# Kernel optimization log

Hardware: AMD Instinct MI355X
Metric: run time of the kernel (lower is better)

Reference implementation:

```python
import jax, jax.numpy as jnp
import numpy as np

HEADS = 8
DIM_HEAD = 64
SCALE = DIM_HEAD ** -0.5


def setup_inputs() -> dict:
    key = jax.random.key(0)
    ks = jax.random.split(key, 8)
    B, Nq, Nk, D = 4, 1024, 2048, 512
    inner = HEADS * DIM_HEAD  # 512
    x = jax.random.normal(ks[0], (B, Nq, D), dtype=jnp.float32)
    context = jax.random.normal(ks[1], (B, Nk, D), dtype=jnp.float32)
    bias = jax.random.normal(ks[2], (B, Nq, Nk), dtype=jnp.float32)
    s = D ** -0.5
    Wq = jax.random.normal(ks[3], (inner, D), dtype=jnp.float32) * s
    Wk = jax.random.normal(ks[4], (inner, D), dtype=jnp.float32) * s
    Wv = jax.random.normal(ks[5], (inner, D), dtype=jnp.float32) * s
    Wo = jax.random.normal(ks[6], (D, inner), dtype=jnp.float32) * s
    bo = jnp.zeros((D,), dtype=jnp.float32)
    return {"x": x, "context": context, "bias": bias,
            "Wq": Wq, "Wk": Wk, "Wv": Wv, "Wo": Wo, "bo": bo}


def reference(x, context, bias, Wq, Wk, Wv, Wo, bo):
    B, Nq, _ = x.shape
    # torch Linear: y = x @ W.T ; reshape (h d) -> b h n d
    q = (x @ Wq.T).reshape(B, Nq, HEADS, DIM_HEAD).transpose(0, 2, 1, 3)
    k = (context @ Wk.T).reshape(B, -1, HEADS, DIM_HEAD).transpose(0, 2, 1, 3)
    v = (context @ Wv.T).reshape(B, -1, HEADS, DIM_HEAD).transpose(0, 2, 1, 3)
    # explicit-score fallback path (bias supplied)
    scores = jnp.einsum('bhqd,bhkd->bhqk', q, k) * SCALE
    scores = scores + bias[:, None, :, :]  # 3D bias -> (B,1,Nq,Nk)
    attn = jax.nn.softmax(scores, axis=-1)
    out = jnp.einsum('bhqk,bhkd->bhqd', attn, v)
    out = out.transpose(0, 2, 1, 3).reshape(B, Nq, HEADS * DIM_HEAD)
    return out @ Wo.T + bo
```

## Files before the change

kernel.cpp:

```cpp
#include <hip/hip_runtime.h>

#define H 8
#define DH 64
#define NQ 1024
#define NK 2048
#define DIN 512
#define B 4
#define KSPLIT 4
#define KRANGE (NK / KSPLIT)
#define KTILES (KRANGE / 64)
#define BHNQ (B * H * NQ)

typedef __bf16 bf16;
typedef __bf16 bf16x8 __attribute__((ext_vector_type(8)));
typedef __bf16 bf16x4 __attribute__((ext_vector_type(4)));
typedef float floatx4 __attribute__((ext_vector_type(4)));

__device__ inline void gload16(const void* g, void* l) {
  __builtin_amdgcn_global_load_lds(
      (const __attribute__((address_space(1))) void*)g,
      (__attribute__((address_space(3))) void*)l, 16, 0, 0);
}

__global__ void cvt_w(const float* __restrict__ wq, const float* __restrict__ wk,
                      const float* __restrict__ wv, const float* __restrict__ wo,
                      bf16* wqb, bf16* wkb, bf16* wvb, bf16* wob) {
  int i = (blockIdx.x * 256 + threadIdx.x) * 4;
  const float* s; bf16* d; int o;
  if (i < 262144)      { s = wq; d = wqb; o = i; }
  else if (i < 524288) { s = wk; d = wkb; o = i - 262144; }
  else if (i < 786432) { s = wv; d = wvb; o = i - 524288; }
  else                 { s = wo; d = wob; o = i - 786432; }
  float4 f = *(const float4*)(s + o);
  bf16x4 v = { (bf16)f.x, (bf16)f.y, (bf16)f.z, (bf16)f.w };
  *(bf16x4*)(d + o) = v;
}

__global__ __launch_bounds__(256) void gemm_qkv(
    const float* __restrict__ x, const float* __restrict__ ctx,
    const bf16* __restrict__ wqb, const bf16* __restrict__ wkb, const bf16* __restrict__ wvb,
    bf16* __restrict__ qb, bf16* __restrict__ kb, bf16* __restrict__ vtb) {
  const int which = blockIdx.z;
  if (which == 0 && blockIdx.y >= 64) return;
  const float* A32 = (which == 0) ? x : ctx;
  const bf16* W = (which == 0) ? wqb : ((which == 1) ? wkb : wvb);
  bf16* outb = (which == 0) ? qb : ((which == 1) ? kb : vtb);
  const int logT = (which == 0) ? 10 : 11;
  const float scale = (which == 0) ? 0.125f : 1.0f;
  const bool vmode = (which == 2);

  __shared__ bf16 Al[2][64 * 32];
  __shared__ bf16 Bl[2][128 * 32];
  const int t = threadIdx.x;
  const int lane = t & 63, w = t >> 6;
  const int ln = lane & 15, quad = lane >> 4;
  const int wm = (w >> 1) * 32, wn = (w & 1) * 64;
  const int rowBase = blockIdx.y * 64;
  const int colBase = blockIdx.x * 128;

  floatx4 acc[2][4] = {};
  const int rA = t >> 2, oA = (t & 3) * 8;
  const int c0 = t, c1 = t + 256;
  const int rB0 = c0 >> 2, oB0 = (c0 & 3) * 8;
  const int rB1 = c1 >> 2, oB1 = (c1 & 3) * 8;
  const float* Ab = A32 + (size_t)(rowBase + rA) * DIN + oA;
  const bf16* Wb = W + (size_t)colBase * DIN;

  float4 la0, la1;
  la0 = *(const float4*)(Ab + 0);
  la1 = *(const float4*)(Ab + 4);
  {
    bf16x8 v = {(bf16)la0.x, (bf16)la0.y, (bf16)la0.z, (bf16)la0.w,
                (bf16)la1.x, (bf16)la1.y, (bf16)la1.z, (bf16)la1.w};
    *(bf16x8*)&Al[0][t * 8] = v;
  }
  gload16(Wb + (size_t)rB0 * DIN + oB0, &Bl[0][c0 * 8]);
  gload16(Wb + (size_t)rB1 * DIN + oB1, &Bl[0][c1 * 8]);
  __syncthreads();

  for (int kk = 0; kk < 16; kk++) {
    const int cur = kk & 1, nxt = cur ^ 1;
    const int k1 = (kk + 1) * 32;
    if (kk < 15) {
      la0 = *(const float4*)(Ab + k1);
      la1 = *(const float4*)(Ab + k1 + 4);
      gload16(Wb + (size_t)rB0 * DIN + k1 + oB0, &Bl[nxt][c0 * 8]);
      gload16(Wb + (size_t)rB1 * DIN + k1 + oB1, &Bl[nxt][c1 * 8]);
    }
    bf16x8 af[2], bfr[4];
#pragma unroll
    for (int i = 0; i < 2; i++)
      af[i] = *(const bf16x8*)&Al[cur][(wm + i * 16 + ln) * 32 + quad * 8];
#pragma unroll
    for (int j = 0; j < 4; j++)
      bfr[j] = *(const bf16x8*)&Bl[cur][(wn + j * 16 + ln) * 32 + quad * 8];
    if (!vmode) {
#pragma unroll
      for (int i = 0; i < 2; i++)
#pragma unroll
        for (int j = 0; j < 4; j++)
          acc[i][j] = __builtin_amdgcn_mfma_f32_16x16x32_bf16(af[i], bfr[j], acc[i][j], 0, 0, 0);
    } else {
#pragma unroll
      for (int i = 0; i < 2; i++)
#pragma unroll
        for (int j = 0; j < 4; j++)
          acc[i][j] = __builtin_amdgcn_mfma_f32_16x16x32_bf16(bfr[j], af[i], acc[i][j], 0, 0, 0);
    }
    if (kk < 15) {
      bf16x8 v = {(bf16)la0.x, (bf16)la0.y, (bf16)la0.z, (bf16)la0.w,
                  (bf16)la1.x, (bf16)la1.y, (bf16)la1.z, (bf16)la1.w};
      *(bf16x8*)&Al[nxt][t * 8] = v;
    }
    __syncthreads();
  }

  const int T = 1 << logT;
#pragma unroll
  for (int i = 0; i < 2; i++)
#pragma unroll
    for (int j = 0; j < 4; j++)
#pragma unroll
      for (int r = 0; r < 4; r++) {
        if (!vmode) {
          const int m = rowBase + wm + i * 16 + quad * 4 + r;
          const int n = colBase + wn + j * 16 + ln;
          const float v = acc[i][j][r] * scale;
          const int bb = m >> logT, tok = m & (T - 1);
          const int hh = n >> 6, d = n & 63;
          outb[((((size_t)(bb * H + hh)) << logT) + tok) * DH + d] = (bf16)v;
        } else {
          const int dg = colBase + wn + j * 16 + quad * 4 + r;
          const int m = rowBase + wm + i * 16 + ln;
          const int bb = m >> logT, tok = m & (T - 1);
          const int hh = dg >> 6, d = dg & 63;
          outb[(((size_t)(bb * H + hh) * DH + d) << logT) + tok] = (bf16)acc[i][j][r];
        }
      }
}

__global__ __launch_bounds__(128) void attn_fwd(
    const bf16* __restrict__ q, const bf16* __restrict__ k,
    const bf16* __restrict__ vt, const float* __restrict__ bias,
    bf16* __restrict__ opb, float* __restrict__ lpart) {
  __shared__ bf16 KL[64 * 64];
  __shared__ bf16 VL[64 * 64];
  __shared__ bf16 Pl[2][2][16 * 64];
  const int tid = threadIdx.x;
  const int lane = tid & 63, w = tid >> 6;
  const int ln = lane & 15, quad = lane >> 4;
  const int hh = blockIdx.y;
  const int b = blockIdx.z >> 2, ks = blockIdx.z & 3;
  const int q0 = blockIdx.x * 64;
  const int k0 = ks * KRANGE;
  const size_t bh = (size_t)b * H + hh;
  const bf16* qp = q + bh * NQ * DH;
  const bf16* kp = k + bh * NK * DH;
  const bf16* vp = vt + bh * DH * NK;
  const float* bp = bias + ((size_t)b * NQ + q0 + w * 32 + quad * 4) * NK + ln;

  bf16x8 qf[2][2];
#pragma unroll
  for (int s = 0; s < 2; s++)
#pragma unroll
    for (int kc = 0; kc < 2; kc++)
      qf[s][kc] = *(const bf16x8*)(qp + (size_t)(q0 + w * 32 + s * 16 + ln) * DH + kc * 32 + quad * 8);

  floatx4 o[2][4] = {};
  floatx4 lac[2] = {};
  const bf16x8 ones = {(bf16)1.f, (bf16)1.f, (bf16)1.f, (bf16)1.f,
                       (bf16)1.f, (bf16)1.f, (bf16)1.f, (bf16)1.f};
  constexpr float L2E = 1.44269504f;
  constexpr float OFF = 34.6246810f;

  for (int tt = 0; tt < KTILES; tt++) {
    const int nk0 = k0 + tt * 64;
#pragma unroll
    for (int s = 0; s < 4; s++) {
      const int i = s * 128 + tid;
      const int sr = i >> 3, sc = (i & 7) ^ (sr & 7);
      gload16(kp + (size_t)(nk0 + sr) * DH + sc * 8, &KL[i * 8]);
      gload16(vp + (size_t)sr * NK + nk0 + sc * 8, &VL[i * 8]);
    }
    float bc[2][4][4];
#pragma unroll
    for (int s = 0; s < 2; s++)
#pragma unroll
      for (int j = 0; j < 4; j++)
#pragma unroll
        for (int r = 0; r < 4; r++)
          bc[s][j][r] = bp[(size_t)(s * 16 + r) * NK + nk0 + j * 16];
    __syncthreads();

    floatx4 s4[2][4];
#pragma unroll
    for (int s = 0; s < 2; s++)
#pragma unroll
      for (int j = 0; j < 4; j++) {
        s4[s][j][0] = bc[s][j][0]; s4[s][j][1] = bc[s][j][1];
        s4[s][j][2] = bc[s][j][2]; s4[s][j][3] = bc[s][j][3];
      }
#pragma unroll
    for (int j = 0; j < 4; j++)
#pragma unroll
      for (int kc = 0; kc < 2; kc++) {
        const int kr = j * 16 + ln;
        bf16x8 kf = *(const bf16x8*)&KL[kr * 64 + (((kc * 4 + quad) ^ (kr & 7)) * 8)];
        s4[0][j] = __builtin_amdgcn_mfma_f32_16x16x32_bf16(qf[0][kc], kf, s4[0][j], 0, 0, 0);
        s4[1][j] = __builtin_amdgcn_mfma_f32_16x16x32_bf16(qf[1][kc], kf, s4[1][j], 0, 0, 0);
      }

#pragma unroll
    for (int s = 0; s < 2; s++)
#pragma unroll
      for (int j = 0; j < 4; j++)
#pragma unroll
        for (int r = 0; r < 4; r++)
          s4[s][j][r] = exp2f(fmaf(s4[s][j][r], L2E, -OFF));

#pragma unroll
    for (int s = 0; s < 2; s++)
#pragma unroll
      for (int j = 0; j < 4; j++)
#pragma unroll
        for (int r = 0; r < 4; r++) {
          const int m = quad * 4 + r;
          Pl[w][s][m * 64 + (((j * 2 + (ln >> 3)) ^ (m & 7)) * 8) + (ln & 7)] = (bf16)s4[s][j][r];
        }
    asm volatile("s_waitcnt lgkmcnt(0)" ::: "memory");
    bf16x8 pf[2][2];
#pragma unroll
    for (int s = 0; s < 2; s++)
#pragma unroll
      for (int kc = 0; kc < 2; kc++)
        pf[s][kc] = *(const bf16x8*)&Pl[w][s][ln * 64 + (((kc * 4 + quad) ^ (ln & 7)) * 8)];

#pragma unroll
    for (int s = 0; s < 2; s++)
#pragma unroll
      for (int kc = 0; kc < 2; kc++)
        lac[s] = __builtin_amdgcn_mfma_f32_16x16x32_bf16(pf[s][kc], ones, lac[s], 0, 0, 0);

#pragma unroll
    for (int jn = 0; jn < 4; jn++)
#pragma unroll
      for (int kc = 0; kc < 2; kc++) {
        const int vr = jn * 16 + ln;
        bf16x8 vf = *(const bf16x8*)&VL[vr * 64 + (((kc * 4 + quad) ^ (vr & 7)) * 8)];
        o[0][jn] = __builtin_amdgcn_mfma_f32_16x16x32_bf16(pf[0][kc], vf, o[0][jn], 0, 0, 0);
        o[1][jn] = __builtin_amdgcn_mfma_f32_16x16x32_bf16(pf[1][kc], vf, o[1][jn], 0, 0, 0);
      }
    __syncthreads();
  }

#pragma unroll
  for (int s = 0; s < 2; s++) {
    bf16* op = opb + (size_t)ks * B * NQ * DIN +
               ((size_t)b * NQ + q0 + w * 32 + s * 16 + quad * 4) * DIN + hh * 64 + ln;
#pragma unroll
    for (int jn = 0; jn < 4; jn++)
#pragma unroll
      for (int r = 0; r < 4; r++)
        op[(size_t)r * DIN + jn * 16] = (bf16)o[s][jn][r];
    if (ln == 0) {
      float4 lv = {lac[s][0], lac[s][1], lac[s][2], lac[s][3]};
      *(float4*)&lpart[((size_t)ks * B * H + b * H + hh) * NQ + q0 + w * 32 + s * 16 + quad * 4] = lv;
    }
  }
}

__global__ __launch_bounds__(256) void gemm_out(
    const bf16* __restrict__ opb, const float* __restrict__ lp,
    const bf16* __restrict__ W, float* __restrict__ outf, const float* __restrict__ bo) {
  __shared__ bf16 Al[2][64 * 32];
  __shared__ bf16 Bl[2][128 * 32];
  const int t = threadIdx.x;
  const int lane = t & 63, w = t >> 6;
  const int ln = lane & 15, quad = lane >> 4;
  const int wm = (w >> 1) * 32, wn = (w & 1) * 64;
  const int rowBase = blockIdx.y * 64;
  const int colBase = blockIdx.x * 128;

  floatx4 acc[2][4] = {};
  const int rA = t >> 2, oA = (t & 3) * 8;
  const int c0 = t, c1 = t + 256;
  const int rB0 = c0 >> 2, oB0 = (c0 & 3) * 8;
  const int rB1 = c1 >> 2, oB1 = (c1 & 3) * 8;
  const int m0 = rowBase + rA;
  const bf16* Wb = W + (size_t)colBase * DIN;

  float linv0[8];
#pragma unroll
  for (int h = 0; h < 8; h++) {
    const int i0 = ((m0 >> 10) * H + h) * NQ + (m0 & 1023);
    linv0[h] = 1.0f / (lp[i0] + lp[BHNQ + i0] + lp[2 * BHNQ + i0] + lp[3 * BHNQ + i0]);
  }

#define STAGE_A(K0V, BUF)                                                      \
  {                                                                            \
    const float sA = linv0[(K0V) >> 6];                                        \
    const size_t base = (size_t)m0 * DIN + (K0V) + oA;                         \
    bf16x8 u0 = *(const bf16x8*)(opb + base);                                  \
    bf16x8 u1 = *(const bf16x8*)(opb + (size_t)B * NQ * DIN + base);           \
    bf16x8 u2 = *(const bf16x8*)(opb + (size_t)2 * B * NQ * DIN + base);       \
    bf16x8 u3 = *(const bf16x8*)(opb + (size_t)3 * B * NQ * DIN + base);       \
    bf16x8 v0;                                                                 \
    _Pragma("unroll")                                                          \
    for (int e = 0; e < 8; e++)                                                \
      v0[e] = (bf16)((((float)u0[e] + (float)u1[e]) +                          \
                      ((float)u2[e] + (float)u3[e])) * sA);                    \
    *(bf16x8*)&Al[BUF][t * 8] = v0;                                            \
  }

  STAGE_A(0, 0);
  gload16(Wb + (size_t)rB0 * DIN + oB0, &Bl[0][c0 * 8]);
  gload16(Wb + (size_t)rB1 * DIN + oB1, &Bl[0][c1 * 8]);
  __syncthreads();

#pragma unroll
  for (int kk = 0; kk < 16; kk++) {
    const int cur = kk & 1, nxt = cur ^ 1;
    if (kk < 15) {
      const int k1 = (kk + 1) * 32;
      STAGE_A(k1, nxt);
      gload16(Wb + (size_t)rB0 * DIN + k1 + oB0, &Bl[nxt][c0 * 8]);
      gload16(Wb + (size_t)rB1 * DIN + k1 + oB1, &Bl[nxt][c1 * 8]);
    }
    bf16x8 af[2], bfr[4];
#pragma unroll
    for (int i = 0; i < 2; i++)
      af[i] = *(const bf16x8*)&Al[cur][(wm + i * 16 + ln) * 32 + quad * 8];
#pragma unroll
    for (int j = 0; j < 4; j++)
      bfr[j] = *(const bf16x8*)&Bl[cur][(wn + j * 16 + ln) * 32 + quad * 8];
#pragma unroll
    for (int i = 0; i < 2; i++)
#pragma unroll
      for (int j = 0; j < 4; j++)
        acc[i][j] = __builtin_amdgcn_mfma_f32_16x16x32_bf16(af[i], bfr[j], acc[i][j], 0, 0, 0);
    __syncthreads();
  }
#undef STAGE_A

#pragma unroll
  for (int i = 0; i < 2; i++)
#pragma unroll
    for (int j = 0; j < 4; j++)
#pragma unroll
      for (int r = 0; r < 4; r++) {
        const int m = rowBase + wm + i * 16 + quad * 4 + r;
        const int n = colBase + wn + j * 16 + ln;
        outf[(size_t)m * DIN + n] = acc[i][j][r] + bo[n];
      }
}

extern "C" void kernel_launch(void* const* d_in, const int* in_sizes, int n_in,
                              void* d_out, int out_size, void* d_ws, size_t ws_size,
                              hipStream_t stream) {
  const float* x    = (const float*)d_in[0];
  const float* ctx  = (const float*)d_in[1];
  const float* bias = (const float*)d_in[2];
  const float* Wq   = (const float*)d_in[3];
  const float* Wk   = (const float*)d_in[4];
  const float* Wv   = (const float*)d_in[5];
  const float* Wo   = (const float*)d_in[6];
  const float* bo   = (const float*)d_in[7];
  float* out = (float*)d_out;

  char* p = (char*)d_ws;
  bf16* wqb  = (bf16*)(p + 0);
  bf16* wkb  = (bf16*)(p + 524288);
  bf16* wvb  = (bf16*)(p + 1048576);
  bf16* wob  = (bf16*)(p + 1572864);
  bf16* qb   = (bf16*)(p + 2097152);
  bf16* kb   = (bf16*)(p + 6291456);
  bf16* vtb  = (bf16*)(p + 14680064);
  bf16* opb  = (bf16*)(p + 23068672);
  float* lpart = (float*)(p + 39845888);

  cvt_w<<<1024, 256, 0, stream>>>(Wq, Wk, Wv, Wo, wqb, wkb, wvb, wob);
  gemm_qkv<<<dim3(4, 128, 3), 256, 0, stream>>>(x, ctx, wqb, wkb, wvb, qb, kb, vtb);
  attn_fwd<<<dim3(NQ / 64, H, B * KSPLIT), 128, 0, stream>>>(qb, kb, vtb, bias, opb, lpart);
  gemm_out<<<dim3(4, 64), 256, 0, stream>>>(opb, lpart, wob, out, bo);
}
```

Before: 208.4 us.

## Fuse K/V projections, halve attention k-split, transpose score MFMA, shrink out-GEMM tiles

Several changes land together. The QKV GEMM computes K and V in one block that shares the staged context tile, so the context fp32 loads and conversion happen once instead of twice. The attention kernel goes from four to two k-splits, and its score MFMA operands are swapped so each lane reads bias as contiguous float4 and writes P as packed bf16x4 with a new swizzle. The output GEMM now uses 32-row tiles and only merges two partial results, which doubles its block count. The trade-offs are fewer attention blocks, less parallelism per row, and more register pressure in the fused K/V GEMM.

```diff
diff --git a/kernel.cpp b/kernel.cpp
--- a/kernel.cpp
+++ b/kernel.cpp
@@ -6,7 +6,7 @@
 #define NK 2048
 #define DIN 512
 #define B 4
-#define KSPLIT 4
+#define KSPLIT 2
 #define KRANGE (NK / KSPLIT)
 #define KTILES (KRANGE / 64)
 #define BHNQ (B * H * NQ)
@@ -43,14 +43,10 @@
   const int which = blockIdx.z;
   if (which == 0 && blockIdx.y >= 64) return;
   const float* A32 = (which == 0) ? x : ctx;
-  const bf16* W = (which == 0) ? wqb : ((which == 1) ? wkb : wvb);
-  bf16* outb = (which == 0) ? qb : ((which == 1) ? kb : vtb);
-  const int logT = (which == 0) ? 10 : 11;
-  const float scale = (which == 0) ? 0.125f : 1.0f;
-  const bool vmode = (which == 2);
 
   __shared__ bf16 Al[2][64 * 32];
-  __shared__ bf16 Bl[2][128 * 32];
+  __shared__ bf16 BlK[2][128 * 32];
+  __shared__ bf16 BlV[2][128 * 32];
   const int t = threadIdx.x;
   const int lane = t & 63, w = t >> 6;
   const int ln = lane & 15, quad = lane >> 4;
@@ -59,12 +55,14 @@
   const int colBase = blockIdx.x * 128;
 
   floatx4 acc[2][4] = {};
+  floatx4 accV[2][4] = {};
   const int rA = t >> 2, oA = (t & 3) * 8;
   const int c0 = t, c1 = t + 256;
   const int rB0 = c0 >> 2, oB0 = (c0 & 3) * 8;
   const int rB1 = c1 >> 2, oB1 = (c1 & 3) * 8;
   const float* Ab = A32 + (size_t)(rowBase + rA) * DIN + oA;
-  const bf16* Wb = W + (size_t)colBase * DIN;
+  const bf16* WbK = ((which == 0) ? wqb : wkb) + (size_t)colBase * DIN;
+  const bf16* WbV = wvb + (size_t)colBase * DIN;
 
   float4 la0, la1;
   la0 = *(const float4*)(Ab + 0);
@@ -74,8 +72,12 @@
                 (bf16)la1.x, (bf16)la1.y, (bf16)la1.z, (bf16)la1.w};
     *(bf16x8*)&Al[0][t * 8] = v;
   }
-  gload16(Wb + (size_t)rB0 * DIN + oB0, &Bl[0][c0 * 8]);
-  gload16(Wb + (size_t)rB1 * DIN + oB1, &Bl[0][c1 * 8]);
+  gload16(WbK + (size_t)rB0 * DIN + oB0, &BlK[0][c0 * 8]);
+  gload16(WbK + (size_t)rB1 * DIN + oB1, &BlK[0][c1 * 8]);
+  if (which == 1) {
+    gload16(WbV + (size_t)rB0 * DIN + oB0, &BlV[0][c0 * 8]);
+    gload16(WbV + (size_t)rB1 * DIN + oB1, &BlV[0][c1 * 8]);
+  }
   __syncthreads();
 
   for (int kk = 0; kk < 16; kk++) {
@@ -84,28 +86,35 @@
     if (kk < 15) {
       la0 = *(const float4*)(Ab + k1);
       la1 = *(const float4*)(Ab + k1 + 4);
-      gload16(Wb + (size_t)rB0 * DIN + k1 + oB0, &Bl[nxt][c0 * 8]);
-      gload16(Wb + (size_t)rB1 * DIN + k1 + oB1, &Bl[nxt][c1 * 8]);
-    }
-    bf16x8 af[2], bfr[4];
+      gload16(WbK + (size_t)rB0 * DIN + k1 + oB0, &BlK[nxt][c0 * 8]);
+      gload16(WbK + (size_t)rB1 * DIN + k1 + oB1, &BlK[nxt][c1 * 8]);
+      if (which == 1) {
+        gload16(WbV + (size_t)rB0 * DIN + k1 + oB0, &BlV[nxt][c0 * 8]);
+        gload16(WbV + (size_t)rB1 * DIN + k1 + oB1, &BlV[nxt][c1 * 8]);
+      }
+    }
+    bf16x8 af[2], bk[4];
 #pragma unroll
     for (int i = 0; i < 2; i++)
       af[i] = *(const bf16x8*)&Al[cur][(wm + i * 16 + ln) * 32 + quad * 8];
 #pragma unroll
     for (int j = 0; j < 4; j++)
-      bfr[j] = *(const bf16x8*)&Bl[cur][(wn + j * 16 + ln) * 32 + quad * 8];
-    if (!vmode) {
+      bk[j] = *(const bf16x8*)&BlK[cur][(wn + j * 16 + ln) * 32 + quad * 8];
+#pragma unroll
+    for (int i = 0; i < 2; i++)
+#pragma unroll
+      for (int j = 0; j < 4; j++)
+        acc[i][j] = __builtin_amdgcn_mfma_f32_16x16x32_bf16(af[i], bk[j], acc[i][j], 0, 0, 0);
+    if (which == 1) {
+      bf16x8 bv[4];
+#pragma unroll
+      for (int j = 0; j < 4; j++)
+        bv[j] = *(const bf16x8*)&BlV[cur][(wn + j * 16 + ln) * 32 + quad * 8];
 #pragma unroll
       for (int i = 0; i < 2; i++)
 #pragma unroll
         for (int j = 0; j < 4; j++)
-          acc[i][j] = __builtin_amdgcn_mfma_f32_16x16x32_bf16(af[i], bfr[j], acc[i][j], 0, 0, 0);
-    } else {
-#pragma unroll
-      for (int i = 0; i < 2; i++)
-#pragma unroll
-        for (int j = 0; j < 4; j++)
-          acc[i][j] = __builtin_amdgcn_mfma_f32_16x16x32_bf16(bfr[j], af[i], acc[i][j], 0, 0, 0);
+          accV[i][j] = __builtin_amdgcn_mfma_f32_16x16x32_bf16(bv[j], af[i], accV[i][j], 0, 0, 0);
     }
     if (kk < 15) {
       bf16x8 v = {(bf16)la0.x, (bf16)la0.y, (bf16)la0.z, (bf16)la0.w,
@@ -115,28 +124,36 @@
     __syncthreads();
   }
 
-  const int T = 1 << logT;
-#pragma unroll
-  for (int i = 0; i < 2; i++)
-#pragma unroll
-    for (int j = 0; j < 4; j++)
-#pragma unroll
-      for (int r = 0; r < 4; r++) {
-        if (!vmode) {
+  if (which == 0) {
+#pragma unroll
+    for (int i = 0; i < 2; i++)
+#pragma unroll
+      for (int j = 0; j < 4; j++)
+#pragma unroll
+        for (int r = 0; r < 4; r++) {
           const int m = rowBase + wm + i * 16 + quad * 4 + r;
           const int n = colBase + wn + j * 16 + ln;
-          const float v = acc[i][j][r] * scale;
-          const int bb = m >> logT, tok = m & (T - 1);
-          const int hh = n >> 6, d = n & 63;
-          outb[((((size_t)(bb * H + hh)) << logT) + tok) * DH + d] = (bf16)v;
-        } else {
+          const int bb = m >> 10, tok = m & 1023;
+          qb[((((size_t)(bb * H + (n >> 6))) << 10) + tok) * DH + (n & 63)] =
+              (bf16)(acc[i][j][r] * 0.125f);
+        }
+  } else {
+#pragma unroll
+    for (int i = 0; i < 2; i++)
+#pragma unroll
+      for (int j = 0; j < 4; j++)
+#pragma unroll
+        for (int r = 0; r < 4; r++) {
+          const int m = rowBase + wm + i * 16 + quad * 4 + r;
+          const int n = colBase + wn + j * 16 + ln;
+          const int bb = m >> 11, tok = m & 2047;
+          kb[((((size_t)(bb * H + (n >> 6))) << 11) + tok) * DH + (n & 63)] = (bf16)acc[i][j][r];
           const int dg = colBase + wn + j * 16 + quad * 4 + r;
-          const int m = rowBase + wm + i * 16 + ln;
-          const int bb = m >> logT, tok = m & (T - 1);
-          const int hh = dg >> 6, d = dg & 63;
-          outb[(((size_t)(bb * H + hh) * DH + d) << logT) + tok] = (bf16)acc[i][j][r];
+          const int mv = rowBase + wm + i * 16 + ln;
+          const int bv2 = mv >> 11, tokv = mv & 2047;
+          vtb[(((size_t)(bv2 * H + (dg >> 6)) * DH + (dg & 63)) << 11) + tokv] = (bf16)accV[i][j][r];
         }
-      }
+  }
 }
 
 __global__ __launch_bounds__(128) void attn_fwd(
@@ -150,14 +167,14 @@
   const int lane = tid & 63, w = tid >> 6;
   const int ln = lane & 15, quad = lane >> 4;
   const int hh = blockIdx.y;
-  const int b = blockIdx.z >> 2, ks = blockIdx.z & 3;
+  const int b = blockIdx.z >> 1, ks = blockIdx.z & 1;
   const int q0 = blockIdx.x * 64;
   const int k0 = ks * KRANGE;
   const size_t bh = (size_t)b * H + hh;
   const bf16* qp = q + bh * NQ * DH;
   const bf16* kp = k + bh * NK * DH;
   const bf16* vp = vt + bh * DH * NK;
-  const float* bp = bias + ((size_t)b * NQ + q0 + w * 32 + quad * 4) * NK + ln;
+  const float* bp = bias + ((size_t)b * NQ + q0 + w * 32 + ln) * NK + quad * 4;
 
   bf16x8 qf[2][2];
 #pragma unroll
@@ -182,14 +199,12 @@
       gload16(kp + (size_t)(nk0 + sr) * DH + sc * 8, &KL[i * 8]);
       gload16(vp + (size_t)sr * NK + nk0 + sc * 8, &VL[i * 8]);
     }
-    float bc[2][4][4];
-#pragma unroll
-    for (int s = 0; s < 2; s++)
-#pragma unroll
-      for (int j = 0; j < 4; j++)
-#pragma unroll
-        for (int r = 0; r < 4; r++)
-          bc[s][j][r] = bp[(size_t)(s * 16 + r) * NK + nk0 + j * 16];
+    float4 bc[2][4];
+#pragma unroll
+    for (int s = 0; s < 2; s++)
+#pragma unroll
+      for (int j = 0; j < 4; j++)
+        bc[s][j] = *(const float4*)(bp + (size_t)(s * 16) * NK + nk0 + j * 16);
     __syncthreads();
 
     floatx4 s4[2][4];
@@ -197,8 +212,8 @@
     for (int s = 0; s < 2; s++)
 #pragma unroll
       for (int j = 0; j < 4; j++) {
-        s4[s][j][0] = bc[s][j][0]; s4[s][j][1] = bc[s][j][1];
-        s4[s][j][2] = bc[s][j][2]; s4[s][j][3] = bc[s][j][3];
+        s4[s][j][0] = bc[s][j].x; s4[s][j][1] = bc[s][j].y;
+        s4[s][j][2] = bc[s][j].z; s4[s][j][3] = bc[s][j].w;
       }
 #pragma unroll
     for (int j = 0; j < 4; j++)
@@ -206,8 +221,8 @@
       for (int kc = 0; kc < 2; kc++) {
         const int kr = j * 16 + ln;
         bf16x8 kf = *(const bf16x8*)&KL[kr * 64 + (((kc * 4 + quad) ^ (kr & 7)) * 8)];
-        s4[0][j] = __builtin_amdgcn_mfma_f32_16x16x32_bf16(qf[0][kc], kf, s4[0][j], 0, 0, 0);
-        s4[1][j] = __builtin_amdgcn_mfma_f32_16x16x32_bf16(qf[1][kc], kf, s4[1][j], 0, 0, 0);
+        s4[0][j] = __builtin_amdgcn_mfma_f32_16x16x32_bf16(kf, qf[0][kc], s4[0][j], 0, 0, 0);
+        s4[1][j] = __builtin_amdgcn_mfma_f32_16x16x32_bf16(kf, qf[1][kc], s4[1][j], 0, 0, 0);
       }
 
 #pragma unroll
@@ -221,19 +236,18 @@
 #pragma unroll
     for (int s = 0; s < 2; s++)
 #pragma unroll
-      for (int j = 0; j < 4; j++)
-#pragma unroll
-        for (int r = 0; r < 4; r++) {
-          const int m = quad * 4 + r;
-          Pl[w][s][m * 64 + (((j * 2 + (ln >> 3)) ^ (m & 7)) * 8) + (ln & 7)] = (bf16)s4[s][j][r];
-        }
+      for (int j = 0; j < 4; j++) {
+        bf16x4 pk = {(bf16)s4[s][j][0], (bf16)s4[s][j][1],
+                     (bf16)s4[s][j][2], (bf16)s4[s][j][3]};
+        *(bf16x4*)&Pl[w][s][ln * 64 + (((j * 4 + quad) ^ (ln & 6)) * 4)] = pk;
+      }
     asm volatile("s_waitcnt lgkmcnt(0)" ::: "memory");
     bf16x8 pf[2][2];
 #pragma unroll
     for (int s = 0; s < 2; s++)
 #pragma unroll
       for (int kc = 0; kc < 2; kc++)
-        pf[s][kc] = *(const bf16x8*)&Pl[w][s][ln * 64 + (((kc * 4 + quad) ^ (ln & 7)) * 8)];
+        pf[s][kc] = *(const bf16x8*)&Pl[w][s][ln * 64 + (((kc * 8 + quad * 2) ^ (ln & 6)) * 4)];
 
 #pragma unroll
     for (int s = 0; s < 2; s++)
@@ -272,16 +286,16 @@
 __global__ __launch_bounds__(256) void gemm_out(
     const bf16* __restrict__ opb, const float* __restrict__ lp,
     const bf16* __restrict__ W, float* __restrict__ outf, const float* __restrict__ bo) {
-  __shared__ bf16 Al[2][64 * 32];
+  __shared__ bf16 Al[2][32 * 32];
   __shared__ bf16 Bl[2][128 * 32];
   const int t = threadIdx.x;
   const int lane = t & 63, w = t >> 6;
   const int ln = lane & 15, quad = lane >> 4;
-  const int wm = (w >> 1) * 32, wn = (w & 1) * 64;
-  const int rowBase = blockIdx.y * 64;
+  const int wm = (w >> 1) * 16, wn = (w & 1) * 64;
+  const int rowBase = blockIdx.y * 32;
   const int colBase = blockIdx.x * 128;
 
-  floatx4 acc[2][4] = {};
+  floatx4 acc[4] = {};
   const int rA = t >> 2, oA = (t & 3) * 8;
   const int c0 = t, c1 = t + 256;
   const int rB0 = c0 >> 2, oB0 = (c0 & 3) * 8;
@@ -292,23 +306,20 @@
   float linv0[8];
 #pragma unroll
   for (int h = 0; h < 8; h++) {
-    const int i0 = ((m0 >> 10) * H + h) * NQ + (m0 & 1023);
-    linv0[h] = 1.0f / (lp[i0] + lp[BHNQ + i0] + lp[2 * BHNQ + i0] + lp[3 * BHNQ + i0]);
+    const int i0 = (((m0 & 4095) >> 10) * H + h) * NQ + (m0 & 1023);
+    linv0[h] = 1.0f / (lp[i0] + lp[BHNQ + i0]);
   }
 
 #define STAGE_A(K0V, BUF)                                                      \
-  {                                                                            \
+  if (t < 128) {                                                               \
     const float sA = linv0[(K0V) >> 6];                                        \
     const size_t base = (size_t)m0 * DIN + (K0V) + oA;                         \
     bf16x8 u0 = *(const bf16x8*)(opb + base);                                  \
     bf16x8 u1 = *(const bf16x8*)(opb + (size_t)B * NQ * DIN + base);           \
-    bf16x8 u2 = *(const bf16x8*)(opb + (size_t)2 * B * NQ * DIN + base);       \
-    bf16x8 u3 = *(const bf16x8*)(opb + (size_t)3 * B * NQ * DIN + base);       \
     bf16x8 v0;                                                                 \
     _Pragma("unroll")                                                          \
     for (int e = 0; e < 8; e++)                                                \
-      v0[e] = (bf16)((((float)u0[e] + (float)u1[e]) +                          \
-                      ((float)u2[e] + (float)u3[e])) * sA);                    \
+      v0[e] = (bf16)(((float)u0[e] + (float)u1[e]) * sA);                      \
     *(bf16x8*)&Al[BUF][t * 8] = v0;                                            \
   }
 
@@ -326,32 +337,26 @@
       gload16(Wb + (size_t)rB0 * DIN + k1 + oB0, &Bl[nxt][c0 * 8]);
       gload16(Wb + (size_t)rB1 * DIN + k1 + oB1, &Bl[nxt][c1 * 8]);
     }
-    bf16x8 af[2], bfr[4];
-#pragma unroll
-    for (int i = 0; i < 2; i++)
-      af[i] = *(const bf16x8*)&Al[cur][(wm + i * 16 + ln) * 32 + quad * 8];
+    bf16x8 af, bfr[4];
+    af = *(const bf16x8*)&Al[cur][(wm + ln) * 32 + quad * 8];
 #pragma unroll
     for (int j = 0; j < 4; j++)
       bfr[j] = *(const bf16x8*)&Bl[cur][(wn + j * 16 + ln) * 32 + quad * 8];
 #pragma unroll
-    for (int i = 0; i < 2; i++)
-#pragma unroll
-      for (int j = 0; j < 4; j++)
-        acc[i][j] = __builtin_amdgcn_mfma_f32_16x16x32_bf16(af[i], bfr[j], acc[i][j], 0, 0, 0);
+    for (int j = 0; j < 4; j++)
+      acc[j] = __builtin_amdgcn_mfma_f32_16x16x32_bf16(af, bfr[j], acc[j], 0, 0, 0);
     __syncthreads();
   }
 #undef STAGE_A
 
 #pragma unroll
-  for (int i = 0; i < 2; i++)
-#pragma unroll
-    for (int j = 0; j < 4; j++)
-#pragma unroll
-      for (int r = 0; r < 4; r++) {
-        const int m = rowBase + wm + i * 16 + quad * 4 + r;
-        const int n = colBase + wn + j * 16 + ln;
-        outf[(size_t)m * DIN + n] = acc[i][j][r] + bo[n];
-      }
+  for (int j = 0; j < 4; j++)
+#pragma unroll
+    for (int r = 0; r < 4; r++) {
+      const int m = rowBase + wm + quad * 4 + r;
+      const int n = colBase + wn + j * 16 + ln;
+      outf[(size_t)m * DIN + n] = acc[j][r] + bo[n];
+    }
 }
 
 extern "C" void kernel_launch(void* const* d_in, const int* in_sizes, int n_in,
@@ -376,10 +381,10 @@
   bf16* kb   = (bf16*)(p + 6291456);
   bf16* vtb  = (bf16*)(p + 14680064);
   bf16* opb  = (bf16*)(p + 23068672);
-  float* lpart = (float*)(p + 39845888);
+  float* lpart = (float*)(p + 31457280);
 
   cvt_w<<<1024, 256, 0, stream>>>(Wq, Wk, Wv, Wo, wqb, wkb, wvb, wob);
-  gemm_qkv<<<dim3(4, 128, 3), 256, 0, stream>>>(x, ctx, wqb, wkb, wvb, qb, kb, vtb);
+  gemm_qkv<<<dim3(4, 128, 2), 256, 0, stream>>>(x, ctx, wqb, wkb, wvb, qb, kb, vtb);
   attn_fwd<<<dim3(NQ / 64, H, B * KSPLIT), 128, 0, stream>>>(qb, kb, vtb, bias, opb, lpart);
-  gemm_out<<<dim3(4, 64), 256, 0, stream>>>(opb, lpart, wob, out, bo);
-}
+  gemm_out<<<dim3(4, 128), 256, 0, stream>>>(opb, lpart, wob, out, bo);
+}
```

After: 204.2 us. 1.02x faster.
